# Optimization experiments

Hardware: AMD Instinct MI355X
Metric: run time of the kernel (lower is better)

## Reference

```python
import jax, jax.numpy as jnp
import numpy as np
from jax.scipy.linalg import expm

LATENT, HIDDEN, N_PARTS, K = 128, 2048, 128, 2048
OMEGA_DIM, TRANZ_DIM = 9 * N_PARTS, 3 * N_PARTS


def setup_inputs() -> dict:
    key = jax.random.key(0)
    ks = jax.random.split(key, 10)

    def w(k, out_d, in_d):
        # eqx.nn.Linear-style scale ~ 1/sqrt(fan_in)
        return jax.random.normal(k, (out_d, in_d), dtype=jnp.float32) / np.sqrt(in_d)

    return {
        "x_init": jax.random.normal(ks[0], (LATENT, K), dtype=jnp.float32),
        "Wo0": w(ks[1], HIDDEN, LATENT),
        "Wo1": w(ks[2], HIDDEN, HIDDEN),
        "Wo2": w(ks[3], HIDDEN, HIDDEN),
        "Wo3": w(ks[4], OMEGA_DIM, HIDDEN),
        "Wt0": w(ks[5], HIDDEN, LATENT),
        "Wt1": w(ks[6], HIDDEN, HIDDEN),
        "Wt2": w(ks[7], HIDDEN, HIDDEN),
        "Wt3": w(ks[8], TRANZ_DIM, HIDDEN),
    }


def _mlp(weights, x):
    # bias-free MLP, relu on all but last layer; x is (d_in, K)
    for i, W in enumerate(weights):
        x = W @ x
        if i + 1 < len(weights):
            x = jax.nn.relu(x)
    return x


def reference(x_init, Wo0, Wo1, Wo2, Wo3, Wt0, Wt1, Wt2, Wt3):
    omega = _mlp([Wo0, Wo1, Wo2, Wo3], x_init)            # (9n, K)
    n = omega.shape[0] // 9
    k = omega.shape[1]
    # exp_omega 2D branch: vmap over columns, each column -> (n,3,3) expm batch
    mats = omega.T.reshape(k * n, 3, 3)
    R = jax.vmap(expm)(mats).reshape(k, 9 * n)            # (K, 9n)
    rotations = R.T                                        # (9n, K)
    translations = _mlp([Wt0, Wt1, Wt2, Wt3], x_init)     # (3n, K)
    # form_transformations (2D branch): stack translation as a 4th row -> (12n, K)
    rot_r = rotations.reshape(n, 3, 3, k)
    tr_r = translations.reshape(n, 1, 3, k)
    transf = jnp.concatenate([rot_r, tr_r], axis=1).reshape(-1, k)  # (12n, K)
    return (omega, transf, rotations, translations)
```

## Files before the change

kernel.cpp:

```cpp
#include <hip/hip_runtime.h>
#include <stdint.h>


typedef short bf16x8 __attribute__((ext_vector_type(8)));
typedef float f32x4 __attribute__((ext_vector_type(4)));

__device__ __forceinline__ unsigned short f2bf(float f) {
  unsigned int x = __float_as_uint(f);
  unsigned int r = (x + 0x7fffu + ((x >> 16) & 1u)) >> 16;
  return (unsigned short)r;
}

__device__ __forceinline__ void gld_lds16(const void* g, void* l) {
  __builtin_amdgcn_global_load_lds(
      (__attribute__((address_space(1))) void*)(g),
      (__attribute__((address_space(3))) void*)(l),
      16, 0, 0);
}

__global__ void prep_k(const float* __restrict__ x,
                       const float* __restrict__ wo0, const float* __restrict__ wo1,
                       const float* __restrict__ wo2, const float* __restrict__ wo3,
                       const float* __restrict__ wt0, const float* __restrict__ wt1,
                       const float* __restrict__ wt2, const float* __restrict__ wt3,
                       unsigned short* __restrict__ dst, unsigned short* __restrict__ xt) {
  __shared__ float tile[32][33];
  const int b = blockIdx.x;
  const int tid = threadIdx.x;
  if (b >= 9984) {
    const int r = b - 9984;
    const int bx = r & 63, by = r >> 6;
    const int tx = tid & 31, ty = tid >> 5;
#pragma unroll
    for (int i = 0; i < 32; i += 8)
      tile[ty + i][tx] = x[(size_t)(by * 32 + ty + i) * 2048 + bx * 32 + tx];
    __syncthreads();
#pragma unroll
    for (int i = 0; i < 32; i += 8)
      xt[(size_t)(bx * 32 + ty + i) * 128 + by * 32 + tx] = f2bf(tile[tx][ty + i]);
    return;
  }
  int idx = (b * 256 + tid) * 8;
  if (idx >= 20447232) return;
  const float* src;
  int off;
  if (idx < 8650752) {
    if (idx < 262144)       { src = wo0; off = idx; }
    else if (idx < 4456448) { src = wo1; off = idx - 262144; }
    else                    { src = wo2; off = idx - 4456448; }
  } else {
    if (idx < 11010048)      { src = wo3; off = idx - 8650752; }
    else if (idx < 11272192) { src = wt0; off = idx - 11010048; }
    else if (idx < 15466496) { src = wt1; off = idx - 11272192; }
    else if (idx < 19660800) { src = wt2; off = idx - 15466496; }
    else                     { src = wt3; off = idx - 19660800; }
  }
  float4 a = *(const float4*)(src + off);
  float4 c = *(const float4*)(src + off + 4);
  uint4 o;
  o.x = (unsigned)f2bf(a.x) | ((unsigned)f2bf(a.y) << 16);
  o.y = (unsigned)f2bf(a.z) | ((unsigned)f2bf(a.w) << 16);
  o.z = (unsigned)f2bf(c.x) | ((unsigned)f2bf(c.y) << 16);
  o.w = (unsigned)f2bf(c.z) | ((unsigned)f2bf(c.w) << 16);
  *(uint4*)(dst + idx) = o;
}

template <int SWZ>
__global__ __launch_bounds__(256, 2) void gemm_tn(
    const unsigned short* __restrict__ A0, const unsigned short* __restrict__ B0,
    unsigned short* __restrict__ C0, int n0tiles, int ldc0,
    const unsigned short* __restrict__ A1, const unsigned short* __restrict__ B1,
    unsigned short* __restrict__ C1, int ldc1, int K) {
  __shared__ alignas(16) unsigned short Asl[128 * 128];
  __shared__ alignas(16) unsigned short Bsl[128 * 128];

  int mt, yt;
  if (SWZ) {
    int id = blockIdx.x;
    int xcd = id & 7, s = id >> 3;
    mt = ((xcd & 1) << 3) + (s & 7);
    yt = ((xcd >> 1) << 3) + (s >> 3);
  } else {
    mt = blockIdx.x;
    yt = blockIdx.y;
  }

  const unsigned short* A;
  const unsigned short* B;
  unsigned short* C;
  int ldc;
  if (yt < n0tiles) { A = A0; B = B0; C = C0; ldc = ldc0; }
  else { A = A1; B = B1; C = C1; ldc = ldc1; yt -= n0tiles; }

  const unsigned short* Ab = A + (size_t)mt * 128 * K;
  const unsigned short* Bb = B + (size_t)yt * 128 * K;

  const int tid = threadIdx.x;
  const int wave = tid >> 6, lane = tid & 63;
  const int mw = (wave >> 1) * 64, nw = (wave & 1) * 64;
  const int l16 = lane & 15, quad = lane >> 4;

  f32x4 acc[4][4] = {};

  for (int k0 = 0; k0 < K; k0 += 128) {
#pragma unroll
    for (int i = 0; i < 8; ++i) {
      int c = i * 256 + tid;
      int row = c >> 4;
      int l = (c & 15) ^ (row & 15);
      gld_lds16(Ab + (size_t)row * K + k0 + l * 8, &Asl[c * 8]);
      gld_lds16(Bb + (size_t)row * K + k0 + l * 8, &Bsl[c * 8]);
    }
    __syncthreads();

#pragma unroll
    for (int h = 0; h < 4; ++h) {
      bf16x8 af[4], bfr[4];
#pragma unroll
      for (int t = 0; t < 4; ++t) {
        int row = mw + t * 16 + l16;
        int p = (h * 4 + quad) ^ (row & 15);
        af[t] = *(const bf16x8*)&Asl[row * 128 + p * 8];
      }
#pragma unroll
      for (int t = 0; t < 4; ++t) {
        int row = nw + t * 16 + l16;
        int p = (h * 4 + quad) ^ (row & 15);
        bfr[t] = *(const bf16x8*)&Bsl[row * 128 + p * 8];
      }
#pragma unroll
      for (int tm = 0; tm < 4; ++tm)
#pragma unroll
        for (int tn = 0; tn < 4; ++tn)
          acc[tm][tn] = __builtin_amdgcn_mfma_f32_16x16x32_bf16(af[tm], bfr[tn], acc[tm][tn], 0, 0, 0);
    }
    __syncthreads();
  }

  const int mbase = mt * 128 + mw;
  const int nbase = yt * 128 + nw;
#pragma unroll
  for (int tm = 0; tm < 4; ++tm) {
#pragma unroll
    for (int tn = 0; tn < 4; ++tn) {
      int col = nbase + tn * 16 + l16;
      int row0 = mbase + tm * 16 + quad * 4;
#pragma unroll
      for (int r = 0; r < 4; ++r) {
        float v = fmaxf(acc[tm][tn][r], 0.0f);
        C[(size_t)(row0 + r) * ldc + col] = f2bf(v);
      }
    }
  }
}

__device__ __forceinline__ void stage_part8(const unsigned short* Ab,
                                            const unsigned short* Bb,
                                            unsigned short* As, unsigned short* Bs,
                                            int k0, int tid, int part, int K) {
#pragma unroll
  for (int i = part * 2; i < part * 2 + 2; ++i) {
    int c = i * 512 + tid;
    int row = c >> 3, pc = c & 7;
    int l = pc ^ (row & 7);
    gld_lds16(Ab + (size_t)row * K + k0 + l * 8, As + c * 8);
  }
  {
    int c = part * 512 + tid;
    int row = c >> 3, pc = c & 7;
    int l = pc ^ (row & 7);
    gld_lds16(Bb + (size_t)row * K + k0 + l * 8, Bs + c * 8);
  }
}

__device__ __forceinline__ bf16x8 ldfrag8(const unsigned short* S, int row, int p) {
  return *(const bf16x8*)&S[row * 64 + ((p ^ (row & 7)) * 8)];
}

__global__ __launch_bounds__(512, 2) void gemm_tn8(
    const unsigned short* __restrict__ A0, const unsigned short* __restrict__ B0,
    unsigned short* __restrict__ C0,
    const unsigned short* __restrict__ A1, const unsigned short* __restrict__ B1,
    unsigned short* __restrict__ C1, int K) {
  __shared__ alignas(16) unsigned short As[3][256 * 64];
  __shared__ alignas(16) unsigned short Bs[3][128 * 64];

  const int id = blockIdx.x;
  const int xcd = id & 7, s = id >> 3;
  const int mt = s & 7;
  const int ntt = xcd * 4 + (s >> 3);

  const unsigned short* A;
  const unsigned short* B;
  unsigned short* C;
  int ntl;
  if (ntt < 16) { A = A0; B = B0; C = C0; ntl = ntt; }
  else          { A = A1; B = B1; C = C1; ntl = ntt - 16; }

  const unsigned short* Ab = A + (size_t)mt * 256 * K;
  const unsigned short* Bb = B + (size_t)ntl * 128 * K;

  const int tid = threadIdx.x;
  const int wave = tid >> 6, lane = tid & 63;
  const int mw = (wave >> 1) * 64;
  const int nw = (wave & 1) * 64;
  const int l16 = lane & 15, quad = lane >> 4;

  f32x4 acc[4][4] = {};
  const int NT = K >> 6;

  stage_part8(Ab, Bb, As[0], Bs[0], 0, tid, 0, K);
  stage_part8(Ab, Bb, As[0], Bs[0], 0, tid, 1, K);
  stage_part8(Ab, Bb, As[1], Bs[1], 64, tid, 0, K);
  stage_part8(Ab, Bb, As[1], Bs[1], 64, tid, 1, K);
  asm volatile("s_waitcnt vmcnt(6)" ::: "memory");
  __builtin_amdgcn_s_barrier();

  int cur = 0;
  for (int t = 0; t < NT; ++t) {
    asm volatile("" ::: "memory");
    const int nxt2 = t + 2;
    int s2 = cur + 2; if (s2 >= 3) s2 -= 3;
    const int k2 = nxt2 << 6;

    if (nxt2 < NT) stage_part8(Ab, Bb, As[s2], Bs[s2], k2, tid, 0, K);
    bf16x8 a0[4], b0[4];
#pragma unroll
    for (int i = 0; i < 4; ++i) a0[i] = ldfrag8(&As[cur][0], mw + i * 16 + l16, quad);
#pragma unroll
    for (int i = 0; i < 4; ++i) b0[i] = ldfrag8(&Bs[cur][0], nw + i * 16 + l16, quad);
    __builtin_amdgcn_s_barrier();
    __builtin_amdgcn_s_setprio(1);
#pragma unroll
    for (int tm = 0; tm < 4; ++tm)
#pragma unroll
      for (int tn = 0; tn < 4; ++tn)
        acc[tm][tn] = __builtin_amdgcn_mfma_f32_16x16x32_bf16(a0[tm], b0[tn], acc[tm][tn], 0, 0, 0);
    __builtin_amdgcn_s_setprio(0);

    if (nxt2 < NT) stage_part8(Ab, Bb, As[s2], Bs[s2], k2, tid, 1, K);
    bf16x8 a1[4], b1[4];
#pragma unroll
    for (int i = 0; i < 4; ++i) a1[i] = ldfrag8(&As[cur][0], mw + i * 16 + l16, 4 + quad);
#pragma unroll
    for (int i = 0; i < 4; ++i) b1[i] = ldfrag8(&Bs[cur][0], nw + i * 16 + l16, 4 + quad);
    __builtin_amdgcn_s_barrier();
    __builtin_amdgcn_s_setprio(1);
#pragma unroll
    for (int tm = 0; tm < 4; ++tm)
#pragma unroll
      for (int tn = 0; tn < 4; ++tn)
        acc[tm][tn] = __builtin_amdgcn_mfma_f32_16x16x32_bf16(a1[tm], b1[tn], acc[tm][tn], 0, 0, 0);
    __builtin_amdgcn_s_setprio(0);

    if (t + 1 < NT) {
      if (nxt2 < NT) asm volatile("s_waitcnt vmcnt(6)" ::: "memory");
      else           asm volatile("s_waitcnt vmcnt(0)" ::: "memory");
      __builtin_amdgcn_s_barrier();
    }
    ++cur; if (cur >= 3) cur = 0;
  }

  const int mbase = mt * 256 + mw;
  const int nbase = ntl * 128 + nw;
#pragma unroll
  for (int tm = 0; tm < 4; ++tm) {
#pragma unroll
    for (int tn = 0; tn < 4; ++tn) {
      int col = nbase + tn * 16 + l16;
      int row0 = mbase + tm * 16 + quad * 4;
#pragma unroll
      for (int r = 0; r < 4; ++r) {
        float v = fmaxf(acc[tm][tn][r], 0.0f);
        C[(size_t)(row0 + r) * 2048 + col] = f2bf(v);
      }
    }
  }
}

__device__ __forceinline__ void mm3(const float* a, const float* b, float* c) {
#pragma unroll
  for (int r = 0; r < 3; ++r)
#pragma unroll
    for (int cc = 0; cc < 3; ++cc)
      c[r * 3 + cc] = a[r * 3 + 0] * b[0 + cc] + a[r * 3 + 1] * b[3 + cc] + a[r * 3 + 2] * b[6 + cc];
}

__device__ __forceinline__ void expm3(const float* a, float* E) {
  float n1 = 0.f;
#pragma unroll
  for (int c = 0; c < 3; ++c) {
    float s = fabsf(a[c]) + fabsf(a[3 + c]) + fabsf(a[6 + c]);
    n1 = fmaxf(n1, s);
  }
  int s = 0;
  if (n1 > 0.25f) {
    s = (int)ceilf(log2f(n1 * 4.0f));
    if (s < 0) s = 0;
  }
  const float scl = exp2f((float)(-s));
  float As[9];
#pragma unroll
  for (int i = 0; i < 9; ++i) As[i] = a[i] * scl;
  float T[9] = {1, 0, 0, 0, 1, 0, 0, 0, 1};
#pragma unroll
  for (int i = 0; i < 9; ++i) E[i] = T[i];
#pragma unroll
  for (int t = 1; t <= 12; ++t) {
    float Tn[9];
    mm3(T, As, Tn);
    const float inv = 1.0f / (float)t;
#pragma unroll
    for (int i = 0; i < 9; ++i) { T[i] = Tn[i] * inv; E[i] += T[i]; }
  }
  for (int q = 0; q < s; ++q) {
    float Tn[9];
    mm3(E, E, Tn);
#pragma unroll
    for (int i = 0; i < 9; ++i) E[i] = Tn[i];
  }
}

__global__ __launch_bounds__(256, 2) void gemm_l3(
    const unsigned short* __restrict__ Ho, const unsigned short* __restrict__ W9,
    const unsigned short* __restrict__ Ht, const unsigned short* __restrict__ W3,
    float* __restrict__ out) {
  __shared__ alignas(16) char smem[16384 + 39168];
  unsigned short* Asl = (unsigned short*)smem;
  unsigned short* Bsl = (unsigned short*)(smem + 16384);
  float* Cl = (float*)(smem + 16384);

  const int mt = blockIdx.x;
  const int yt = blockIdx.y;
  const int tid = threadIdx.x;
  const int wave = tid >> 6, lane = tid & 63;
  const int l16 = lane & 15, quad = lane >> 4;
  const int mbase = mt * 64;

  float* omega  = out;
  float* transf = out + (size_t)1152 * 2048;
  float* rot    = out + (size_t)(1152 + 1536) * 2048;
  float* transl = out + (size_t)(1152 + 1536 + 1152) * 2048;

  if (yt < 8) {
    const unsigned short* Ab = Ho + (size_t)mbase * 2048;
    const unsigned short* Bb = W9 + (size_t)yt * 144 * 2048;
    const int mw = wave * 16;
    f32x4 acc[9] = {};

    for (int k0 = 0; k0 < 2048; k0 += 128) {
#pragma unroll
      for (int i = 0; i < 4; ++i) {
        int c = i * 256 + tid;
        int row = c >> 4;
        int l = (c & 15) ^ (row & 15);
        gld_lds16(Ab + (size_t)row * 2048 + k0 + l * 8, &Asl[c * 8]);
      }
#pragma unroll
      for (int i = 0; i < 9; ++i) {
        int c = i * 256 + tid;
        int row = c >> 4;
        int l = (c & 15) ^ (row & 15);
        gld_lds16(Bb + (size_t)row * 2048 + k0 + l * 8, &Bsl[c * 8]);
      }
      __syncthreads();
#pragma unroll
      for (int h = 0; h < 4; ++h) {
        bf16x8 af;
        {
          int row = mw + l16;
          int p = (h * 4 + quad) ^ (row & 15);
          af = *(const bf16x8*)&Asl[row * 128 + p * 8];
        }
#pragma unroll
        for (int t = 0; t < 9; ++t) {
          int row = t * 16 + l16;
          int p = (h * 4 + quad) ^ (row & 15);
          bf16x8 bf = *(const bf16x8*)&Bsl[row * 128 + p * 8];
          acc[t] = __builtin_amdgcn_mfma_f32_16x16x32_bf16(af, bf, acc[t], 0, 0, 0);
        }
      }
      __syncthreads();
    }

#pragma unroll
    for (int t = 0; t < 9; ++t) {
      int d = t * 16 + l16;
      int s0 = mw + quad * 4;
      *(f32x4*)&Cl[d * 68 + s0] = acc[t];
    }
    __syncthreads();

    const int jbase = yt * 16;
    const int k = mbase + lane;
#pragma unroll 1
    for (int pp = 0; pp < 4; ++pp) {
      int pl = wave * 4 + pp;
      int j = jbase + pl;
      float a[9];
#pragma unroll
      for (int i = 0; i < 9; ++i) a[i] = Cl[(pl * 9 + i) * 68 + lane];
#pragma unroll
      for (int i = 0; i < 9; ++i) omega[(size_t)(9 * j + i) * 2048 + k] = a[i];
      float E[9];
      expm3(a, E);
#pragma unroll
      for (int i = 0; i < 9; ++i) {
        rot[(size_t)(9 * j + i) * 2048 + k] = E[i];
        transf[(size_t)(12 * j + i) * 2048 + k] = E[i];
      }
    }
  } else {
    const int nt = yt - 8;
    const unsigned short* Ab = Ht + (size_t)mbase * 2048;
    const unsigned short* Bb = W3 + (size_t)nt * 128 * 2048;
    const int mw = (wave >> 1) * 32, nw = (wave & 1) * 64;
    f32x4 acc[2][4] = {};

    for (int k0 = 0; k0 < 2048; k0 += 128) {
#pragma unroll
      for (int i = 0; i < 4; ++i) {
        int c = i * 256 + tid;
        int row = c >> 4;
        int l = (c & 15) ^ (row & 15);
        gld_lds16(Ab + (size_t)row * 2048 + k0 + l * 8, &Asl[c * 8]);
      }
#pragma unroll
      for (int i = 0; i < 8; ++i) {
        int c = i * 256 + tid;
        int row = c >> 4;
        int l = (c & 15) ^ (row & 15);
        gld_lds16(Bb + (size_t)row * 2048 + k0 + l * 8, &Bsl[c * 8]);
      }
      __syncthreads();
#pragma unroll
      for (int h = 0; h < 4; ++h) {
        bf16x8 af[2], bfr[4];
#pragma unroll
        for (int t = 0; t < 2; ++t) {
          int row = mw + t * 16 + l16;
          int p = (h * 4 + quad) ^ (row & 15);
          af[t] = *(const bf16x8*)&Asl[row * 128 + p * 8];
        }
#pragma unroll
        for (int t = 0; t < 4; ++t) {
          int row = nw + t * 16 + l16;
          int p = (h * 4 + quad) ^ (row & 15);
          bfr[t] = *(const bf16x8*)&Bsl[row * 128 + p * 8];
        }
#pragma unroll
        for (int tm = 0; tm < 2; ++tm)
#pragma unroll
          for (int tn = 0; tn < 4; ++tn)
            acc[tm][tn] = __builtin_amdgcn_mfma_f32_16x16x32_bf16(af[tm], bfr[tn], acc[tm][tn], 0, 0, 0);
      }
      __syncthreads();
    }

    const int nbase = nt * 128 + nw;
#pragma unroll
    for (int tm = 0; tm < 2; ++tm) {
#pragma unroll
      for (int tn = 0; tn < 4; ++tn) {
        int n = nbase + tn * 16 + l16;
        int row0 = mbase + mw + tm * 16 + quad * 4;
        int j = n / 3, c = n % 3;
        *(f32x4*)&transl[(size_t)n * 2048 + row0] = acc[tm][tn];
        *(f32x4*)&transf[(size_t)(12 * j + 9 + c) * 2048 + row0] = acc[tm][tn];
      }
    }
  }
}

extern "C" void kernel_launch(void* const* d_in, const int* in_sizes, int n_in,
                              void* d_out, int out_size, void* d_ws, size_t ws_size,
                              hipStream_t stream) {
  const float* x   = (const float*)d_in[0];
  const float* Wo0 = (const float*)d_in[1];
  const float* Wo1 = (const float*)d_in[2];
  const float* Wo2 = (const float*)d_in[3];
  const float* Wo3 = (const float*)d_in[4];
  const float* Wt0 = (const float*)d_in[5];
  const float* Wt1 = (const float*)d_in[6];
  const float* Wt2 = (const float*)d_in[7];
  const float* Wt3 = (const float*)d_in[8];

  unsigned short* wb   = (unsigned short*)d_ws;
  unsigned short* wo0b = wb + 0;
  unsigned short* wo1b = wb + 262144;
  unsigned short* wo2b = wb + 4456448;
  unsigned short* wo3b = wb + 8650752;
  unsigned short* wt0b = wb + 11010048;
  unsigned short* wt1b = wb + 11272192;
  unsigned short* wt2b = wb + 15466496;
  unsigned short* wt3b = wb + 19660800;
  unsigned short* Xt   = wb + 20447232;
  unsigned short* HoA  = Xt + 262144;
  unsigned short* HoB  = HoA + 4194304;
  unsigned short* HtA  = HoB + 4194304;
  unsigned short* HtB  = HtA + 4194304;

  prep_k<<<10240, 256, 0, stream>>>(x, Wo0, Wo1, Wo2, Wo3, Wt0, Wt1, Wt2, Wt3, wb, Xt);

  gemm_tn<1><<<512, 256, 0, stream>>>(Xt, wo0b, HoA, 16, 2048,
                                      Xt, wt0b, HtA, 2048, 128);
  gemm_tn8<<<256, 512, 0, stream>>>(HoA, wo1b, HoB, HtA, wt1b, HtB, 2048);
  gemm_tn8<<<256, 512, 0, stream>>>(HoB, wo2b, HoA, HtB, wt2b, HtA, 2048);
  gemm_l3<<<dim3(32, 11), 256, 0, stream>>>(HoA, wo3b, HtA, wt3b, (float*)d_out);
}
```

Baseline: 281.7 us.

## Switch gemm_tn8 to double-buffered LDS pipeline and route layer 2 to gemm_tn

Replaces the three-stage LDS ring with split staging in gemm_tn8 with a two-slot double buffer. Each iteration stages the whole next tile, then reads all fragments through inline-asm ds_read_b128 with precomputed swizzled offsets and does a full vmcnt(0) wait and barrier once per iteration. Global and LDS addresses are hoisted out of the loop, and the second hidden-layer GEMM is moved to the older gemm_tn<1> kernel. The aim is fewer barriers and less address arithmetic, but prefetch depth is lower, so load latency may be exposed, and the last iteration redundantly reloads the final tile.

```diff
diff --git a/kernel.cpp b/kernel.cpp
--- a/kernel.cpp
+++ b/kernel.cpp
@@ -17,6 +17,21 @@
       (__attribute__((address_space(3))) void*)(l),
       16, 0, 0);
 }
+
+__device__ __forceinline__ unsigned lds_addr(const void* p) {
+  return (unsigned)(uintptr_t)(__attribute__((address_space(3))) const void*)p;
+}
+
+__device__ __forceinline__ bf16x8 ds_read128(unsigned a) {
+  bf16x8 r;
+  asm volatile("ds_read_b128 %0, %1" : "=v"(r) : "v"(a));
+  return r;
+}
+
+#define ASM_BAR asm volatile("s_barrier" ::: "memory")
+#define LGKM0   asm volatile("s_waitcnt lgkmcnt(0)" ::: "memory")
+#define VMCNT0  asm volatile("s_waitcnt vmcnt(0)" ::: "memory")
+#define SCHED0  __builtin_amdgcn_sched_barrier(0)
 
 __global__ void prep_k(const float* __restrict__ x,
                        const float* __restrict__ wo0, const float* __restrict__ wo1,
@@ -154,36 +169,12 @@
   }
 }
 
-__device__ __forceinline__ void stage_part8(const unsigned short* Ab,
-                                            const unsigned short* Bb,
-                                            unsigned short* As, unsigned short* Bs,
-                                            int k0, int tid, int part, int K) {
-#pragma unroll
-  for (int i = part * 2; i < part * 2 + 2; ++i) {
-    int c = i * 512 + tid;
-    int row = c >> 3, pc = c & 7;
-    int l = pc ^ (row & 7);
-    gld_lds16(Ab + (size_t)row * K + k0 + l * 8, As + c * 8);
-  }
-  {
-    int c = part * 512 + tid;
-    int row = c >> 3, pc = c & 7;
-    int l = pc ^ (row & 7);
-    gld_lds16(Bb + (size_t)row * K + k0 + l * 8, Bs + c * 8);
-  }
-}
-
-__device__ __forceinline__ bf16x8 ldfrag8(const unsigned short* S, int row, int p) {
-  return *(const bf16x8*)&S[row * 64 + ((p ^ (row & 7)) * 8)];
-}
-
 __global__ __launch_bounds__(512, 2) void gemm_tn8(
     const unsigned short* __restrict__ A0, const unsigned short* __restrict__ B0,
     unsigned short* __restrict__ C0,
     const unsigned short* __restrict__ A1, const unsigned short* __restrict__ B1,
     unsigned short* __restrict__ C1, int K) {
-  __shared__ alignas(16) unsigned short As[3][256 * 64];
-  __shared__ alignas(16) unsigned short Bs[3][128 * 64];
+  __shared__ alignas(16) unsigned short SM[2 * 16384 + 2 * 8192];
 
   const int id = blockIdx.x;
   const int xcd = id & 7, s = id >> 3;
@@ -206,59 +197,87 @@
   const int nw = (wave & 1) * 64;
   const int l16 = lane & 15, quad = lane >> 4;
 
+  const unsigned short* gA[4];
+  unsigned short* dA[4];
+#pragma unroll
+  for (int i = 0; i < 4; ++i) {
+    int c = i * 512 + tid, row = c >> 3, pc = c & 7, l = pc ^ (row & 7);
+    gA[i] = Ab + (size_t)row * K + l * 8;
+    dA[i] = SM + c * 8;
+  }
+  const unsigned short* gB[2];
+  unsigned short* dB[2];
+#pragma unroll
+  for (int j = 0; j < 2; ++j) {
+    int c = j * 512 + tid, row = c >> 3, pc = c & 7, l = pc ^ (row & 7);
+    gB[j] = Bb + (size_t)row * K + l * 8;
+    dB[j] = SM + 32768 + c * 8;
+  }
+
+  unsigned aoff[2][4], boff[2][4];
+#pragma unroll
+  for (int ph = 0; ph < 2; ++ph)
+#pragma unroll
+    for (int i = 0; i < 4; ++i) {
+      int ra = mw + i * 16 + l16;
+      aoff[ph][i] = (unsigned)(ra * 128 + (((ph * 4 + quad) ^ (ra & 7)) * 16));
+      int rb = nw + i * 16 + l16;
+      boff[ph][i] = (unsigned)(rb * 128 + (((ph * 4 + quad) ^ (rb & 7)) * 16));
+    }
+  const unsigned Au = lds_addr(SM);
+  const unsigned Bu = Au + 65536;
+
   f32x4 acc[4][4] = {};
   const int NT = K >> 6;
 
-  stage_part8(Ab, Bb, As[0], Bs[0], 0, tid, 0, K);
-  stage_part8(Ab, Bb, As[0], Bs[0], 0, tid, 1, K);
-  stage_part8(Ab, Bb, As[1], Bs[1], 64, tid, 0, K);
-  stage_part8(Ab, Bb, As[1], Bs[1], 64, tid, 1, K);
-  asm volatile("s_waitcnt vmcnt(6)" ::: "memory");
-  __builtin_amdgcn_s_barrier();
+  auto STAGE = [&](int slot, int k2) {
+    const int sa = slot * 16384, sb = slot * 8192;
+#pragma unroll
+    for (int i = 0; i < 4; ++i) gld_lds16(gA[i] + k2, dA[i] + sa);
+#pragma unroll
+    for (int j = 0; j < 2; ++j) gld_lds16(gB[j] + k2, dB[j] + sb);
+  };
+
+  STAGE(0, 0);
+  VMCNT0;
+  ASM_BAR;
 
   int cur = 0;
   for (int t = 0; t < NT; ++t) {
-    asm volatile("" ::: "memory");
-    const int nxt2 = t + 2;
-    int s2 = cur + 2; if (s2 >= 3) s2 -= 3;
-    const int k2 = nxt2 << 6;
-
-    if (nxt2 < NT) stage_part8(Ab, Bb, As[s2], Bs[s2], k2, tid, 0, K);
-    bf16x8 a0[4], b0[4];
-#pragma unroll
-    for (int i = 0; i < 4; ++i) a0[i] = ldfrag8(&As[cur][0], mw + i * 16 + l16, quad);
-#pragma unroll
-    for (int i = 0; i < 4; ++i) b0[i] = ldfrag8(&Bs[cur][0], nw + i * 16 + l16, quad);
-    __builtin_amdgcn_s_barrier();
+    const int nxt = cur ^ 1;
+    int k1 = (t + 1) << 6;
+    if (k1 > K - 64) k1 = K - 64;
+    STAGE(nxt, k1);
+
+    const unsigned ab = Au + cur * 32768, bb = Bu + cur * 16384;
+    bf16x8 a0[4], b0[4], a1[4], b1[4];
+#pragma unroll
+    for (int i = 0; i < 4; ++i) a0[i] = ds_read128(ab + aoff[0][i]);
+#pragma unroll
+    for (int i = 0; i < 4; ++i) b0[i] = ds_read128(bb + boff[0][i]);
+#pragma unroll
+    for (int i = 0; i < 4; ++i) a1[i] = ds_read128(ab + aoff[1][i]);
+#pragma unroll
+    for (int i = 0; i < 4; ++i) b1[i] = ds_read128(bb + boff[1][i]);
+    LGKM0;
+    SCHED0;
     __builtin_amdgcn_s_setprio(1);
 #pragma unroll
     for (int tm = 0; tm < 4; ++tm)
 #pragma unroll
       for (int tn = 0; tn < 4; ++tn)
         acc[tm][tn] = __builtin_amdgcn_mfma_f32_16x16x32_bf16(a0[tm], b0[tn], acc[tm][tn], 0, 0, 0);
-    __builtin_amdgcn_s_setprio(0);
-
-    if (nxt2 < NT) stage_part8(Ab, Bb, As[s2], Bs[s2], k2, tid, 1, K);
-    bf16x8 a1[4], b1[4];
-#pragma unroll
-    for (int i = 0; i < 4; ++i) a1[i] = ldfrag8(&As[cur][0], mw + i * 16 + l16, 4 + quad);
-#pragma unroll
-    for (int i = 0; i < 4; ++i) b1[i] = ldfrag8(&Bs[cur][0], nw + i * 16 + l16, 4 + quad);
-    __builtin_amdgcn_s_barrier();
-    __builtin_amdgcn_s_setprio(1);
 #pragma unroll
     for (int tm = 0; tm < 4; ++tm)
 #pragma unroll
       for (int tn = 0; tn < 4; ++tn)
         acc[tm][tn] = __builtin_amdgcn_mfma_f32_16x16x32_bf16(a1[tm], b1[tn], acc[tm][tn], 0, 0, 0);
     __builtin_amdgcn_s_setprio(0);
-
-    if (t + 1 < NT) {
-      if (nxt2 < NT) asm volatile("s_waitcnt vmcnt(6)" ::: "memory");
-      else           asm volatile("s_waitcnt vmcnt(0)" ::: "memory");
-      __builtin_amdgcn_s_barrier();
-    }
-    ++cur; if (cur >= 3) cur = 0;
+    SCHED0;
+
+    VMCNT0;
+    ASM_BAR;
+    cur = nxt;
   }
 
   const int mbase = mt * 256 + mw;
@@ -505,6 +524,7 @@
   gemm_tn<1><<<512, 256, 0, stream>>>(Xt, wo0b, HoA, 16, 2048,
                                       Xt, wt0b, HtA, 2048, 128);
   gemm_tn8<<<256, 512, 0, stream>>>(HoA, wo1b, HoB, HtA, wt1b, HtB, 2048);
-  gemm_tn8<<<256, 512, 0, stream>>>(HoB, wo2b, HoA, HtB, wt2b, HtA, 2048);
+  gemm_tn<1><<<512, 256, 0, stream>>>(HoB, wo2b, HoA, 16, 2048,
+                                      HtB, wt2b, HtA, 2048, 2048);
   gemm_l3<<<dim3(32, 11), 256, 0, stream>>>(HoA, wo3b, HtA, wt3b, (float*)d_out);
 }
```

New measurement: 238.5 us. 15.4% less time.
